# Optimization experiments

Hardware: AMD Instinct MI355X
Metric: run time of the kernel (lower is better)

The kernel has to match this reference:

```python
import jax, jax.numpy as jnp
import numpy as np

N = 50000      # nodes per graph
E = 800000     # edges per graph (avg degree 16)
IN = 128       # in_dim
OUT = 64       # out_dim
HEADS = 2      # second GCNConv out = OUT*HEADS = 128
FILL = 2.0     # improved=True self-loop weight


def setup_inputs():
    key = jax.random.key(0)
    ks = jax.random.split(key, 10)
    x1 = jax.random.normal(ks[0], (N, IN), jnp.float32)
    edge_index1 = jax.random.randint(ks[1], (2, E), 0, N)
    edge_weight1 = jax.random.uniform(ks[2], (E,), jnp.float32)
    x2 = jax.random.normal(ks[3], (N, IN), jnp.float32)
    edge_index2 = jax.random.randint(ks[4], (2, E), 0, N)
    edge_weight2 = jax.random.uniform(ks[5], (E,), jnp.float32)
    # shared tower params (source bug: gcn1 used for both inputs)
    W1 = jax.random.normal(ks[6], (IN, OUT), jnp.float32) / np.sqrt(IN)
    b1 = jnp.zeros((OUT,), jnp.float32)
    W2 = jax.random.normal(ks[7], (OUT, OUT * HEADS), jnp.float32) / np.sqrt(OUT)
    b2 = jnp.zeros((OUT * HEADS,), jnp.float32)
    return {"x1": x1, "edge_index1": edge_index1, "edge_weight1": edge_weight1,
            "x2": x2, "edge_index2": edge_index2, "edge_weight2": edge_weight2,
            "W1": W1, "b1": b1, "W2": W2, "b2": b2}


def _gcn_conv(x, src, dst, ew, W, b, n):
    # GCNConv(improved=True, add_self_loops=True, aggr='max')
    loop = jnp.arange(n)
    src = jnp.concatenate([src, loop])
    dst = jnp.concatenate([dst, loop])
    ew = jnp.concatenate([ew, jnp.full((n,), FILL, ew.dtype)])
    # symmetric gcn normalization
    deg = jax.ops.segment_sum(ew, dst, num_segments=n)
    dinv = jnp.where(deg > 0, jax.lax.rsqrt(jnp.maximum(deg, 1e-30)), 0.0)
    norm = dinv[src] * ew * dinv[dst]          # [E+N]
    h = x @ W                                   # [N, F_out]
    msg = norm[:, None] * h[src]                # [E+N, F_out] gathered messages
    out = jax.ops.segment_max(msg, dst, num_segments=n)  # scatter-max
    out = jnp.where(jnp.isfinite(out), out, 0.0)          # guard empty segments
    return out + b


def _tower(x, ei, ew, W1, b1, W2, b2):
    ew = jax.nn.relu(ew)
    h = _gcn_conv(x, ei[0], ei[1], ew, W1, b1, x.shape[0])
    return _gcn_conv(h, ei[0], ei[1], ew, W2, b2, x.shape[0])


def reference(x1, edge_index1, edge_weight1, x2, edge_index2, edge_weight2, W1, b1, W2, b2):
    g1 = _tower(x1, edge_index1, edge_weight1, W1, b1, W2, b2)
    g2 = _tower(x2, edge_index2, edge_weight2, W1, b1, W2, b2)
    return (g1, g2)
```

## Files before the change

kernel.cpp:

```cpp
#include <hip/hip_runtime.h>
#include <hip/hip_fp16.h>

static constexpr float FILLW = 2.0f;
static constexpr int BSH  = 6;
static constexpr int CAPB = 1792;
static constexpr int NPB  = 256;
static constexpr int EPT  = 8;

__device__ __forceinline__ unsigned pk_mul(unsigned a, unsigned b){
    unsigned r; asm("v_pk_mul_f16 %0, %1, %2" : "=v"(r) : "v"(a), "v"(b)); return r;
}
__device__ __forceinline__ unsigned pk_max(unsigned a, unsigned b){
    unsigned r; asm("v_pk_max_f16 %0, %1, %2" : "=v"(r) : "v"(a), "v"(b)); return r;
}

template<int F, int K, int TR, int KC, bool SCALE, typename OutT>
__device__ __forceinline__ void gemm_tile(const float* __restrict__ A,
        const float* __restrict__ W, OutT* __restrict__ C,
        const float* __restrict__ dv, int rb, int N,
        float* __restrict__ Ws, float* __restrict__ As){
    constexpr int NCH = K / KC;
    constexpr int TRp = TR + 4;
    constexpr int CG  = F / 8;
    constexpr int LPT = TR * KC / 1024;
    const int tid = threadIdx.x;
    for (int i = tid; i < K * F / 4; i += 256)
        ((float4*)Ws)[i] = ((const float4*)W)[i];
    const int tx = tid % CG, ty = tid / CG;
    const int c0 = tx * 8, r0 = ty * 8;

    float acc[8][8];
    #pragma unroll
    for (int i = 0; i < 8; ++i)
        #pragma unroll
        for (int j = 0; j < 8; ++j) acc[i][j] = 0.f;

    float4 st[LPT];
    auto gload = [&](int kc){
        #pragma unroll
        for (int l2 = 0; l2 < LPT; ++l2){
            int l = l2 * 256 + tid;
            int r = l / (KC / 4);
            int kk = (l % (KC / 4)) * 4;
            int ar = rb + r; if (ar >= N) ar = N - 1;
            st[l2] = *(const float4*)(A + (size_t)ar * K + kc * KC + kk);
        }
    };
    auto swrite = [&](int buf){
        float* p = As + buf * (KC * TRp);
        #pragma unroll
        for (int l2 = 0; l2 < LPT; ++l2){
            int l = l2 * 256 + tid;
            int r = l / (KC / 4);
            int kk = (l % (KC / 4)) * 4;
            p[(kk+0)*TRp + r] = st[l2].x;
            p[(kk+1)*TRp + r] = st[l2].y;
            p[(kk+2)*TRp + r] = st[l2].z;
            p[(kk+3)*TRp + r] = st[l2].w;
        }
    };

    gload(0); swrite(0);
    __syncthreads();
    for (int kc = 0; kc < NCH; ++kc){
        if (kc + 1 < NCH) gload(kc + 1);
        const float* Ab = As + (kc & 1) * (KC * TRp);
        #pragma unroll
        for (int j = 0; j < KC; ++j){
            const float* wrow = Ws + (kc * KC + j) * F + c0;
            float4 w0 = *(const float4*)(wrow);
            float4 w1 = *(const float4*)(wrow + 4);
            float4 a0 = *(const float4*)(Ab + j * TRp + r0);
            float4 a1 = *(const float4*)(Ab + j * TRp + r0 + 4);
            float av[8] = {a0.x,a0.y,a0.z,a0.w,a1.x,a1.y,a1.z,a1.w};
            float wvv[8] = {w0.x,w0.y,w0.z,w0.w,w1.x,w1.y,w1.z,w1.w};
            #pragma unroll
            for (int rr = 0; rr < 8; ++rr)
                #pragma unroll
                for (int cc = 0; cc < 8; ++cc)
                    acc[rr][cc] = fmaf(av[rr], wvv[cc], acc[rr][cc]);
        }
        if (kc + 1 < NCH){ swrite((kc + 1) & 1); __syncthreads(); }
    }
    #pragma unroll
    for (int rr = 0; rr < 8; ++rr){
        int row = rb + r0 + rr;
        if (row < N){
            float scv = 1.0f;
            if constexpr (SCALE) scv = dv[row];
            if constexpr (sizeof(OutT) == 2){
                __half2 o2[4];
                #pragma unroll
                for (int q = 0; q < 4; ++q)
                    o2[q] = __floats2half2_rn(acc[rr][2*q]*scv, acc[rr][2*q+1]*scv);
                *(float4*)((__half*)C + (size_t)row * F + c0) = *(float4*)o2;
            } else {
                float4 o0 = {acc[rr][0]*scv, acc[rr][1]*scv, acc[rr][2]*scv, acc[rr][3]*scv};
                float4 o1 = {acc[rr][4]*scv, acc[rr][5]*scv, acc[rr][6]*scv, acc[rr][7]*scv};
                *(float4*)((float*)C + (size_t)row * F + c0)     = o0;
                *(float4*)((float*)C + (size_t)row * F + c0 + 4) = o1;
            }
        }
    }
}

__global__ void __launch_bounds__(256) k_cg1(const float* __restrict__ x0,
        const float* __restrict__ x1, const float* __restrict__ W1,
        __half* __restrict__ h0, __half* __restrict__ h1,
        const int* __restrict__ dst0, const int* __restrict__ dst1,
        int* __restrict__ cnts,
        int N, int E, int BPT, int GB, int B1){
    __shared__ float Ws[64 * 128];
    __shared__ float As[2 * 8 * 260];
    if ((int)blockIdx.x < GB){
        int t  = (int)blockIdx.x / BPT;
        int rb = ((int)blockIdx.x - t * BPT) * 256;
        gemm_tile<64,128,256,8,false,__half>(t ? x1 : x0, W1, t ? h1 : h0,
                                             nullptr, rb, N, Ws, As);
        return;
    }
    int c = (int)blockIdx.x - GB;
    int t = c / NPB, blk = c % NPB;
    const int* dst = t ? dst1 : dst0;
    int* hist = (int*)Ws;
    const int tid = threadIdx.x;
    for (int i = tid; i < B1; i += 256) hist[i] = 0;
    __syncthreads();
    int per = (E + NPB - 1) / NPB;
    int e0 = blk * per;
    int e1 = e0 + per; if (e1 > E) e1 = E;
    for (int e = e0 + tid; e < e1; e += 256 * EPT){
        int dl[EPT];
        #pragma unroll
        for (int q = 0; q < EPT; ++q){ int ee = e + q*256; dl[q] = (ee < e1) ? dst[ee] : -1; }
        #pragma unroll
        for (int q = 0; q < EPT; ++q) if (dl[q] >= 0) atomicAdd(&hist[dl[q] >> BSH], 1);
    }
    __syncthreads();
    int* co = cnts + (size_t)(t * NPB + blk) * B1;
    for (int i = tid; i < B1; i += 256) co[i] = hist[i];
}

__global__ void __launch_bounds__(64) k_scanR(int* __restrict__ cnts,
        int* __restrict__ gcnt, int B1){
    int bid = (int)blockIdx.x;
    int t = bid / B1, b = bid % B1;
    int lane = threadIdx.x;
    int* cp = cnts + (size_t)t * NPB * B1 + b;
    int x[4];
    #pragma unroll
    for (int j = 0; j < 4; ++j) x[j] = cp[(size_t)(lane * 4 + j) * B1];
    int s = x[0] + x[1] + x[2] + x[3];
    int sc = s;
    #pragma unroll
    for (int o = 1; o < 64; o <<= 1){ int u = __shfl_up(sc, o); if (lane >= o) sc += u; }
    int e0 = sc - s;
    int e1 = e0 + x[0], e2 = e1 + x[1], e3 = e2 + x[2];
    cp[(size_t)(lane * 4 + 0) * B1] = e0;
    cp[(size_t)(lane * 4 + 1) * B1] = e1;
    cp[(size_t)(lane * 4 + 2) * B1] = e2;
    cp[(size_t)(lane * 4 + 3) * B1] = e3;
    if (lane == 63) gcnt[t * B1 + b] = sc;
}

__global__ void __launch_bounds__(256) k_scatter(const int* __restrict__ src0,
        const int* __restrict__ src1,
        const int* __restrict__ dst0, const int* __restrict__ dst1,
        const float* __restrict__ ew0, const float* __restrict__ ew1,
        const int* __restrict__ cnts, uint2* __restrict__ stage,
        int N, int E, int B1){
    __shared__ int hist[1024];
    int c = (int)blockIdx.x;
    int t = c / NPB, blk = c % NPB;
    const int* src = t ? src1 : src0;
    const int* dst = t ? dst1 : dst0;
    const float* ew = t ? ew1 : ew0;
    uint2* stg = stage + (size_t)t * B1 * CAPB;
    const int* co = cnts + (size_t)(t * NPB + blk) * B1;
    const int tid = threadIdx.x;
    for (int i = tid; i < B1; i += 256) hist[i] = co[i];
    __syncthreads();
    int per = (E + NPB - 1) / NPB;
    int e0 = blk * per;
    int e1 = e0 + per; if (e1 > E) e1 = E;
    for (int e = e0 + tid; e < e1; e += 256 * EPT){
        int dl[EPT], sl[EPT]; float wl[EPT];
        #pragma unroll
        for (int q = 0; q < EPT; ++q){
            int ee = e + q*256;
            if (ee < e1){ dl[q] = dst[ee]; sl[q] = src[ee]; wl[q] = fmaxf(ew[ee], 0.f); }
            else dl[q] = -1;
        }
        int r[EPT];
        #pragma unroll
        for (int q = 0; q < EPT; ++q)
            if (dl[q] >= 0) r[q] = atomicAdd(&hist[dl[q] >> BSH], 1);
        #pragma unroll
        for (int q = 0; q < EPT; ++q)
            if (dl[q] >= 0 && r[q] < CAPB)
                stg[(size_t)(dl[q] >> BSH) * CAPB + r[q]] =
                    make_uint2(__float_as_uint(wl[q]),
                               (unsigned)sl[q] | ((unsigned)(dl[q] & 63) << 16));
    }
}

__global__ void __launch_bounds__(256) k_pack(const uint2* __restrict__ stage,
        const int* __restrict__ gcnt, int* __restrict__ woff,
        uint2* __restrict__ sn, float* __restrict__ dinv,
        __half* __restrict__ h1, int N, int E, int B1){
    const int bid = (int)blockIdx.x, tid = threadIdx.x;
    const int t = bid / B1, b = bid % B1;
    const uint2* stg = stage + (size_t)t * B1 * CAPB;
    const int* gc = gcnt + t * B1;
    __shared__ int   wsum[4];
    __shared__ int   nh[64];
    __shared__ float nw[64];
    __shared__ int   offs[64];
    __shared__ float dvs[64];
    int acc = 0;
    for (int i = tid; i < b; i += 256) acc += gc[i];
    #pragma unroll
    for (int o = 32; o; o >>= 1) acc += __shfl_down(acc, o);
    int lane = tid & 63, wv = tid >> 6;
    if (lane == 0) wsum[wv] = acc;
    if (tid < 64){ nh[tid] = 0; nw[tid] = 0.f; }
    __syncthreads();
    const int base = wsum[0] + wsum[1] + wsum[2] + wsum[3];
    int cnt = gc[b]; if (cnt > CAPB) cnt = CAPB;

    int   rr[7]; uint2 rec[7];
    #pragma unroll
    for (int q = 0; q < 7; ++q){
        int j = q * 256 + tid;
        if (j < cnt){
            uint2 v = stg[(size_t)b * CAPB + j];
            int nl = (v.y >> 16) & 63;
            rr[q] = atomicAdd(&nh[nl], 1);
            atomicAdd(&nw[nl], __uint_as_float(v.x));
            rec[q] = v;
        } else rec[q].y = 0xFFFFFFFFu;
    }
    __syncthreads();
    if (tid < 64){
        int v = nh[tid], sc = v;
        #pragma unroll
        for (int o = 1; o < 64; o <<= 1){ int u = __shfl_up(sc, o); if (tid >= o) sc += u; }
        offs[tid] = sc - v;
        int n = (b << BSH) + tid;
        float dv = 0.f;
        if (n < N){
            dv = rsqrtf(FILLW + nw[tid]);
            woff[t * N + n] = base + sc - v;
            dinv[t * N + n] = dv;
        }
        dvs[tid] = dv;
    }
    __syncthreads();
    uint2* sno = sn + (size_t)t * E;
    #pragma unroll
    for (int q = 0; q < 7; ++q){
        if (rec[q].y != 0xFFFFFFFFu){
            int nl   = (int)((rec[q].y >> 16) & 63);
            unsigned srcv = rec[q].y & 0xFFFFu;
            __half hw = __float2half(__uint_as_float(rec[q].x));
            unsigned hu = (unsigned)__half_as_ushort(hw);
            sno[(size_t)base + offs[nl] + rr[q]] =
                make_uint2(srcv, hu | (hu << 16));
        }
    }
    __half2* hb = (__half2*)(h1 + ((size_t)t * N + ((size_t)b << BSH)) * 64);
    #pragma unroll
    for (int j = 0; j < 8; ++j){
        int idx = j * 256 + tid;
        int r = idx >> 5, cc = idx & 31;
        if ((b << BSH) + r < N){
            float2 f = __half22float2(hb[r * 32 + cc]);
            float dv = dvs[r];
            hb[r * 32 + cc] = __floats2half2_rn(f.x * dv, f.y * dv);
        }
    }
}

__global__ void __launch_bounds__(256) k_gemm2(const float* __restrict__ A0,
        const float* __restrict__ A1, const float* __restrict__ W,
        __half* __restrict__ C0, __half* __restrict__ C1,
        const float* __restrict__ dinv, int N, int BPT){
    __shared__ float Ws[64 * 128];
    __shared__ float As[2 * 16 * 132];
    int t  = (int)blockIdx.x / BPT;
    int rb = ((int)blockIdx.x - t * BPT) * 128;
    gemm_tile<128,64,128,16,true,__half>(t ? A1 : A0, W, t ? C1 : C0,
                                         dinv + t * N, rb, N, Ws, As);
}

template<int F, int UG>
__global__ void __launch_bounds__(256) k_agg(const int* __restrict__ woff,
        const uint2* __restrict__ sn, const float* __restrict__ dinv,
        const __half* __restrict__ H0, const __half* __restrict__ H1,
        const float* __restrict__ bias, float* __restrict__ O0, float* __restrict__ O1,
        int N, int E, int BPT){
    constexpr int LPR = F / 8;
    constexpr int EG  = 64 / LPR;
    const int t = (int)blockIdx.x / BPT;
    const int lane = threadIdx.x & 63, wv = threadIdx.x >> 6;
    int n = ((int)blockIdx.x - t * BPT) * 4 + wv;
    if (n >= N) return;
    int g = t * N + n;
    int beg = woff[g];
    int end = (n == N - 1) ? E : woff[g + 1];
    int cnt = end - beg;
    const uint2* st = sn + (size_t)t * E;
    const __half* H = t ? H1 : H0;
    float* O = t ? O1 : O0;
    const int fl = lane % LPR;
    const int eg = lane / LPR;

    unsigned acc[4];
    {
        float4 hv = *(const float4*)(H + (size_t)n * F + fl * 8);
        const unsigned* hp = (const unsigned*)&hv;
        const unsigned two2 = 0x40004000u;
        #pragma unroll
        for (int k = 0; k < 4; ++k) acc[k] = pk_mul(hp[k], two2);
    }
    for (int base = 0; base < cnt; base += 64){
        int m = cnt - base; if (m > 64) m = 64;
        uint2 er = make_uint2(0u, 0u);
        if (lane < m) er = st[beg + base + lane];
        int es = (int)er.x;
        int ep = (int)er.y;
        for (int j = 0; j < m; j += EG * UG){
            int sl[UG], wl[UG]; float4 hv[UG];
            #pragma unroll
            for (int u = 0; u < UG; ++u){
                int jj = j + u * EG + eg; if (jj > m - 1) jj = m - 1;
                sl[u] = __shfl(es, jj);
                wl[u] = __shfl(ep, jj);
            }
            #pragma unroll
            for (int u = 0; u < UG; ++u)
                hv[u] = *(const float4*)(H + (size_t)sl[u] * F + fl * 8);
            #pragma unroll
            for (int u = 0; u < UG; ++u){
                const unsigned* hp = (const unsigned*)&hv[u];
                unsigned w2 = (unsigned)wl[u];
                #pragma unroll
                for (int k = 0; k < 4; ++k)
                    acc[k] = pk_max(acc[k], pk_mul(hp[k], w2));
            }
        }
    }
    #pragma unroll
    for (int msk = LPR; msk < 64; msk <<= 1)
        #pragma unroll
        for (int k = 0; k < 4; ++k){
            unsigned o = (unsigned)__shfl_xor((int)acc[k], msk);
            acc[k] = pk_max(acc[k], o);
        }
    float di = dinv[g];
    if constexpr (F == 128){
        int f0 = fl * 8 + eg * 2;
        float2 f = __half22float2(*(__half2*)&acc[eg]);
        float2 bb = *(const float2*)(bias + f0);
        *(float2*)(O + (size_t)n * F + f0) =
            make_float2(di * f.x + bb.x, di * f.y + bb.y);
    } else {
        int f0 = fl * 8 + eg;
        unsigned av = acc[eg >> 1];
        unsigned short hs = (unsigned short)((eg & 1) ? (av >> 16) : (av & 0xFFFFu));
        float v = __half2float(__ushort_as_half(hs));
        O[(size_t)n * F + f0] = di * v + bias[f0];
    }
}


extern "C" void kernel_launch(void* const* d_in, const int* in_sizes, int n_in,
                              void* d_out, int out_size, void* d_ws, size_t ws_size,
                              hipStream_t stream){
    const int E  = in_sizes[2];
    const int F1 = in_sizes[7];
    const int F2 = in_sizes[9];
    const int IN = in_sizes[6] / F1;
    const int N  = in_sizes[0] / IN;
    const int B1 = (N + 63) >> BSH;

    const float* W1 = (const float*)d_in[6];
    const float* b1 = (const float*)d_in[7];
    const float* W2 = (const float*)d_in[8];
    const float* b2 = (const float*)d_in[9];

    auto need = [&](int G){
        return (size_t)G * E * 8
             + (size_t)G * N * F2 * 2
             + (size_t)G * N * F1 * 4
             + (size_t)G * N * 8
             + (size_t)G * B1 * 4
             + (size_t)G * NPB * B1 * 4
             + 4096;
    };
    const int G = (ws_size >= need(2)) ? 2 : 1;

    uint2*  sn    = (uint2*)d_ws;
    __half* hbuf  = (__half*)(sn + (size_t)G * E);
    float*  out1  = (float*)(hbuf + (size_t)G * N * F2);
    uint2*  stage = (uint2*)out1;
    float*  dinv  = out1 + (size_t)G * N * F1;
    int*    woff  = (int*)(dinv + (size_t)G * N);
    int*    gcnt  = woff + (size_t)G * N;
    int*    cnts  = gcnt + (size_t)G * B1;

    const int BPT1 = (N + 255) / 256;
    const int BPT2 = (N + 127) / 128;
    const int ABT  = (N + 3) / 4;
    const int GB   = G * BPT1;

    for (int it = 0; it < 2; it += G){
        int t0 = it, t1 = (G == 2) ? it + 1 : it;
        const float* x0 = (const float*)d_in[t0*3], * x1 = (const float*)d_in[t1*3];
        const int* ei0 = (const int*)d_in[t0*3+1], * ei1 = (const int*)d_in[t1*3+1];
        const float* ew0 = (const float*)d_in[t0*3+2], * ew1 = (const float*)d_in[t1*3+2];
        const int* src0 = ei0, * dst0 = ei0 + E;
        const int* src1 = ei1, * dst1 = ei1 + E;
        __half* h1_0 = hbuf, * h1_1 = hbuf + (size_t)(G-1) * N * F1;
        __half* h2_0 = hbuf, * h2_1 = hbuf + (size_t)(G-1) * N * F2;
        float* o1_0 = out1, * o1_1 = out1 + (size_t)(G-1) * N * F1;
        float* go0 = (float*)d_out + (size_t)t0 * N * F2;
        float* go1 = (float*)d_out + (size_t)t1 * N * F2;

        k_cg1<<<GB + G * NPB, 256, 0, stream>>>(x0, x1, W1, h1_0, h1_1,
                                                dst0, dst1, cnts, N, E, BPT1, GB, B1);
        k_scanR<<<G * B1, 64, 0, stream>>>(cnts, gcnt, B1);
        k_scatter<<<G * NPB, 256, 0, stream>>>(src0, src1, dst0, dst1, ew0, ew1,
                                               cnts, stage, N, E, B1);
        k_pack<<<G * B1, 256, 0, stream>>>(stage, gcnt, woff, sn, dinv, hbuf, N, E, B1);
        k_agg<64,4><<<G * ABT, 256, 0, stream>>>(woff, sn, dinv, h1_0, h1_1, b1,
                                                 o1_0, o1_1, N, E, ABT);
        k_gemm2<<<G * BPT2, 256, 0, stream>>>(o1_0, o1_1, W2, h2_0, h2_1, dinv, N, BPT2);
        k_agg<128,4><<<G * ABT, 256, 0, stream>>>(woff, sn, dinv, h2_0, h2_1, b2,
                                                  go0, go1, N, E, ABT);
    }
}
```

Before: 339.9 us.

## Map graph towers to XCD halves and raise layer-1 aggregation unroll

Remaps block indices so that, when both graphs run together, blocks of graph 0 go to XCDs 0-3 and blocks of graph 1 go to XCDs 4-7 (round-robin dispatch with c&7). The partition, scatter, pack and aggregation kernels all use this mapping, so each graph's data stays within one group of XCD L2 caches instead of being spread across all eight. It also raises the layer-1 aggregation unroll (UG) from 4 to 8 and moves the dinv load earlier. The grid is padded to a multiple of 8, which adds a few idle blocks, and a bounds check is added in pack.

```diff
diff --git a/kernel.cpp b/kernel.cpp
--- a/kernel.cpp
+++ b/kernel.cpp
@@ -104,12 +104,18 @@
     }
 }
 
+__device__ __forceinline__ void xcd_map(int c, int TW2, int LIN_BPT,
+                                        int& t, int& chunk){
+    if (TW2){ int x = c & 7; t = x >> 2; chunk = (c >> 3) * 4 + (x & 3); }
+    else    { t = c / LIN_BPT; chunk = c - t * LIN_BPT; }
+}
+
 __global__ void __launch_bounds__(256) k_cg1(const float* __restrict__ x0,
         const float* __restrict__ x1, const float* __restrict__ W1,
         __half* __restrict__ h0, __half* __restrict__ h1,
         const int* __restrict__ dst0, const int* __restrict__ dst1,
         int* __restrict__ cnts,
-        int N, int E, int BPT, int GB, int B1){
+        int N, int E, int BPT, int GB, int B1, int TW2){
     __shared__ float Ws[64 * 128];
     __shared__ float As[2 * 8 * 260];
     if ((int)blockIdx.x < GB){
@@ -119,8 +125,8 @@
                                              nullptr, rb, N, Ws, As);
         return;
     }
-    int c = (int)blockIdx.x - GB;
-    int t = c / NPB, blk = c % NPB;
+    int t, blk;
+    xcd_map((int)blockIdx.x - GB, TW2, NPB, t, blk);
     const int* dst = t ? dst1 : dst0;
     int* hist = (int*)Ws;
     const int tid = threadIdx.x;
@@ -168,10 +174,10 @@
         const int* __restrict__ dst0, const int* __restrict__ dst1,
         const float* __restrict__ ew0, const float* __restrict__ ew1,
         const int* __restrict__ cnts, uint2* __restrict__ stage,
-        int N, int E, int B1){
+        int N, int E, int B1, int TW2){
     __shared__ int hist[1024];
-    int c = (int)blockIdx.x;
-    int t = c / NPB, blk = c % NPB;
+    int t, blk;
+    xcd_map((int)blockIdx.x, TW2, NPB, t, blk);
     const int* src = t ? src1 : src0;
     const int* dst = t ? dst1 : dst0;
     const float* ew = t ? ew1 : ew0;
@@ -207,9 +213,11 @@
 __global__ void __launch_bounds__(256) k_pack(const uint2* __restrict__ stage,
         const int* __restrict__ gcnt, int* __restrict__ woff,
         uint2* __restrict__ sn, float* __restrict__ dinv,
-        __half* __restrict__ h1, int N, int E, int B1){
-    const int bid = (int)blockIdx.x, tid = threadIdx.x;
-    const int t = bid / B1, b = bid % B1;
+        __half* __restrict__ h1, int N, int E, int B1, int TW2){
+    int t, b;
+    xcd_map((int)blockIdx.x, TW2, B1, t, b);
+    if (b >= B1) return;
+    const int tid = threadIdx.x;
     const uint2* stg = stage + (size_t)t * B1 * CAPB;
     const int* gc = gcnt + t * B1;
     __shared__ int   wsum[4];
@@ -298,16 +306,18 @@
         const uint2* __restrict__ sn, const float* __restrict__ dinv,
         const __half* __restrict__ H0, const __half* __restrict__ H1,
         const float* __restrict__ bias, float* __restrict__ O0, float* __restrict__ O1,
-        int N, int E, int BPT){
+        int N, int E, int BPT, int TW2){
     constexpr int LPR = F / 8;
     constexpr int EG  = 64 / LPR;
-    const int t = (int)blockIdx.x / BPT;
     const int lane = threadIdx.x & 63, wv = threadIdx.x >> 6;
-    int n = ((int)blockIdx.x - t * BPT) * 4 + wv;
+    int t, chunk;
+    xcd_map((int)blockIdx.x, TW2, BPT, t, chunk);
+    int n = chunk * 4 + wv;
     if (n >= N) return;
     int g = t * N + n;
     int beg = woff[g];
     int end = (n == N - 1) ? E : woff[g + 1];
+    float di = dinv[g];
     int cnt = end - beg;
     const uint2* st = sn + (size_t)t * E;
     const __half* H = t ? H1 : H0;
@@ -357,7 +367,6 @@
             unsigned o = (unsigned)__shfl_xor((int)acc[k], msk);
             acc[k] = pk_max(acc[k], o);
         }
-    float di = dinv[g];
     if constexpr (F == 128){
         int f0 = fl * 8 + eg * 2;
         float2 f = __half22float2(*(__half2*)&acc[eg]);
@@ -399,6 +408,7 @@
              + 4096;
     };
     const int G = (ws_size >= need(2)) ? 2 : 1;
+    const int TW2 = (G == 2);
 
     uint2*  sn    = (uint2*)d_ws;
     __half* hbuf  = (__half*)(sn + (size_t)G * E);
@@ -413,6 +423,9 @@
     const int BPT2 = (N + 127) / 128;
     const int ABT  = (N + 3) / 4;
     const int GB   = G * BPT1;
+    const int partGrid = TW2 ? (NPB / 4) * 8          : G * NPB;
+    const int packGrid = TW2 ? ((B1 + 3) / 4) * 8     : G * B1;
+    const int aggGrid  = TW2 ? ((ABT + 3) / 4) * 8    : G * ABT;
 
     for (int it = 0; it < 2; it += G){
         int t0 = it, t1 = (G == 2) ? it + 1 : it;
@@ -427,16 +440,17 @@
         float* go0 = (float*)d_out + (size_t)t0 * N * F2;
         float* go1 = (float*)d_out + (size_t)t1 * N * F2;
 
-        k_cg1<<<GB + G * NPB, 256, 0, stream>>>(x0, x1, W1, h1_0, h1_1,
-                                                dst0, dst1, cnts, N, E, BPT1, GB, B1);
+        k_cg1<<<GB + partGrid, 256, 0, stream>>>(x0, x1, W1, h1_0, h1_1,
+                                                 dst0, dst1, cnts, N, E, BPT1, GB, B1, TW2);
         k_scanR<<<G * B1, 64, 0, stream>>>(cnts, gcnt, B1);
-        k_scatter<<<G * NPB, 256, 0, stream>>>(src0, src1, dst0, dst1, ew0, ew1,
-                                               cnts, stage, N, E, B1);
-        k_pack<<<G * B1, 256, 0, stream>>>(stage, gcnt, woff, sn, dinv, hbuf, N, E, B1);
-        k_agg<64,4><<<G * ABT, 256, 0, stream>>>(woff, sn, dinv, h1_0, h1_1, b1,
-                                                 o1_0, o1_1, N, E, ABT);
+        k_scatter<<<partGrid, 256, 0, stream>>>(src0, src1, dst0, dst1, ew0, ew1,
+                                                cnts, stage, N, E, B1, TW2);
+        k_pack<<<packGrid, 256, 0, stream>>>(stage, gcnt, woff, sn, dinv, hbuf,
+                                             N, E, B1, TW2);
+        k_agg<64,8><<<aggGrid, 256, 0, stream>>>(woff, sn, dinv, h1_0, h1_1, b1,
+                                                 o1_0, o1_1, N, E, ABT, TW2);
         k_gemm2<<<G * BPT2, 256, 0, stream>>>(o1_0, o1_1, W2, h2_0, h2_1, dinv, N, BPT2);
-        k_agg<128,4><<<G * ABT, 256, 0, stream>>>(woff, sn, dinv, h2_0, h2_1, b2,
-                                                  go0, go1, N, E, ABT);
-    }
-}
+        k_agg<128,4><<<aggGrid, 256, 0, stream>>>(woff, sn, dinv, h2_0, h2_1, b2,
+                                                  go0, go1, N, E, ABT, TW2);
+    }
+}
```

After: 349.0 us. 2.7% more time.
